# Performance work log

Hardware: AMD Instinct MI355X
Metric: run time of the kernel (lower is better)

The kernel has to match this reference:

```python
import jax, jax.numpy as jnp
import numpy as np

# Static config (matches init_kwargs)
B, T, D = 4, 2048, 1024
E = 8            # num_experts
K = 2            # top_k
S = 1            # num_shared_experts
H = 1408         # expert_hidden_dim = round_to(4*1024//(K+S), 64)
N = B * T        # 8192 tokens
CAPACITY = 2560  # ceil(1.25 * K * N / E)
AUX_COEF = 0.01


def setup_inputs() -> dict:
    key = jax.random.key(0)
    ks = jax.random.split(key, 6)
    s = 1024 ** -0.5
    return {
        "x": jax.random.normal(ks[0], (B, T, D), jnp.float32),
        "router_weight": jax.random.normal(ks[1], (E, D), jnp.float32) * 0.02,
        "w_fc": jax.random.normal(ks[2], (E, D, H), jnp.float32) * s,
        "w_proj": jax.random.normal(ks[3], (E, H, D), jnp.float32) * s,
        "ws_fc": jax.random.normal(ks[4], (S, D, H), jnp.float32) * s,
        "ws_proj": jax.random.normal(ks[5], (S, H, D), jnp.float32) * s,
    }


def reference(x, router_weight, w_fc, w_proj, ws_fc, ws_proj):
    x_flat = x.reshape(N, D)

    # Shared experts: relu(x @ ws_fc)^2 @ ws_proj, summed over S experts
    h_s = jnp.square(jax.nn.relu(jnp.einsum("nd,sdh->snh", x_flat, ws_fc)))
    shared_out = jnp.einsum("snh,shd->nd", h_s, ws_proj)

    # Router: softmax in fp32, top-k, renormalize
    router_logits = x_flat @ router_weight.T                 # [N, E]
    routing_probs = jax.nn.softmax(router_logits.astype(jnp.float32), axis=-1)
    topk_probs, topk_idx = jax.lax.top_k(routing_probs, K)   # [N, K]
    topk_probs = topk_probs / (jnp.sum(topk_probs, axis=-1, keepdims=True) + 1e-9)
    topk_probs = topk_probs.astype(x.dtype)

    # Aux load-balancing loss (f uses top-1 assignment, no grad)
    f = jax.lax.stop_gradient(
        jnp.mean(jax.nn.one_hot(topk_idx[:, 0], E, dtype=routing_probs.dtype), axis=0))
    p = jnp.mean(routing_probs, axis=0)
    aux_loss = AUX_COEF * float(E) * jnp.sum(f * p)

    # Capacity-based dispatch: stable sort assignments by expert id
    flat_idx = topk_idx.reshape(-1)                          # [N*K]
    flat_probs = topk_probs.reshape(-1)                      # [N*K]
    flat_tok = jnp.repeat(jnp.arange(N, dtype=jnp.int32), K)  # [N*K]
    order = jnp.argsort(flat_idx, stable=True)
    sorted_idx = flat_idx[order]
    sorted_tok = flat_tok[order]
    sorted_probs = flat_probs[order]

    counts = jnp.zeros((E,), jnp.int32).at[flat_idx].add(1)
    starts = jnp.concatenate([jnp.zeros((1,), jnp.int32), jnp.cumsum(counts[:-1])])
    pos_within = jnp.arange(N * K, dtype=jnp.int32) - starts[sorted_idx]
    keep = (pos_within < CAPACITY).astype(x.dtype)
    pos_clamped = jnp.minimum(pos_within, CAPACITY - 1)
    slot = sorted_idx * CAPACITY + pos_clamped               # [N*K] -> E*CAPACITY buffer

    # Scatter tokens into per-expert capacity buffers (dropped tokens zeroed by keep)
    expert_inputs = jnp.zeros((E * CAPACITY, D), x.dtype).at[slot].add(
        x_flat[sorted_tok] * keep[:, None])
    expert_inputs = expert_inputs.reshape(E, CAPACITY, D)

    # Grouped expert FFN: relu(.)^2 MLP per expert
    hidden = jnp.square(jax.nn.relu(jnp.einsum("ecd,edh->ech", expert_inputs, w_fc)))
    expert_output = jnp.einsum("ech,ehd->ecd", hidden, w_proj).reshape(E * CAPACITY, D)

    # Gather + weighted scatter-combine back to tokens
    gathered = expert_output[slot]                           # [N*K, D]
    weighted = gathered * (sorted_probs * keep)[:, None]
    routed_out = jnp.zeros((N, D), x.dtype).at[sorted_tok].add(weighted)

    y = (routed_out + shared_out).reshape(B, T, D)
    return y, aux_loss
```

## Files before the change

### kernel.cpp

```cpp
#include <hip/hip_runtime.h>


#define NTOK 8192
#define DDIM 1024
#define HDIM 1408
#define CAP  2560
#define NROWS (NTOK + 8*CAP)
#define YN   8388608

typedef __bf16 bf16x8 __attribute__((ext_vector_type(8)));
typedef float  f32x4  __attribute__((ext_vector_type(4)));

typedef __attribute__((address_space(1))) void gvoid_t;
typedef __attribute__((address_space(3))) void svoid_t;

static __device__ __forceinline__ void load_lds16(const void* g, void* l) {
  __builtin_amdgcn_global_load_lds((gvoid_t*)g, (svoid_t*)l, 16, 0, 0);
}

__global__ __launch_bounds__(256) void zero_kernel(float* __restrict__ y) {
  size_t idx = (size_t)blockIdx.x * 256 + threadIdx.x;
  float4 z = make_float4(0.f, 0.f, 0.f, 0.f);
  float4* p = (float4*)y;
#pragma unroll
  for (int j = 0; j < 4; ++j) p[idx + (size_t)j * 524288] = z;
}

__global__ __launch_bounds__(256) void tconv2_kernel(
    const float* __restrict__ in, __bf16* __restrict__ out,
    const float* __restrict__ in_s, __bf16* __restrict__ out_s, int R, int C) {
  __shared__ float t[64][33];
  int z = blockIdx.z, tid = threadIdx.x;
  const float* ip = (z < 8) ? in + (size_t)z * R * C : in_s;
  __bf16* op = (z < 8) ? out + (size_t)z * R * C : out_s;
  int c0 = blockIdx.x * 32, r0 = blockIdx.y * 64;
  int tx = tid & 31, ty = tid >> 5;
#pragma unroll
  for (int k = 0; k < 8; ++k)
    t[ty + k * 8][tx] = ip[(size_t)(r0 + ty + k * 8) * C + c0 + tx];
  __syncthreads();
  int cl = tid >> 3, rq = (tid & 7) * 8;
  bf16x8 o;
#pragma unroll
  for (int j = 0; j < 8; ++j) o[j] = (__bf16)t[rq + j][cl];
  *(bf16x8*)(op + (size_t)(c0 + cl) * R + r0 + rq) = o;
}

__global__ __launch_bounds__(256) void router_kernel(
    const float* __restrict__ x, const float* __restrict__ rw,
    __bf16* __restrict__ xbf,
    int2* __restrict__ e01, float2* __restrict__ p01,
    int* __restrict__ tok_row, float* __restrict__ scale_row,
    float* __restrict__ psum_part, int* __restrict__ fcnt_part) {
  __shared__ float rwl[8 * 1024];
  __shared__ float ps[8];
  __shared__ int fc[8];
  int tid = threadIdx.x;
  if (tid < 8) { ps[tid] = 0.f; fc[tid] = 0; }
  float4* rl4 = (float4*)rwl;
  const float4* rg4 = (const float4*)rw;
#pragma unroll
  for (int j = 0; j < 8; ++j) rl4[tid + 256 * j] = rg4[tid + 256 * j];
  __syncthreads();
  int lane = tid & 63, wid = tid >> 6;
  for (int it = 0; it < 8; ++it) {
    int t = blockIdx.x * 32 + wid * 8 + it;
    const float4* xt = (const float4*)(x + (size_t)t * DDIM);
    float a[8];
#pragma unroll
    for (int e = 0; e < 8; ++e) a[e] = 0.f;
    float4 v[4];
#pragma unroll
    for (int jj = 0; jj < 4; ++jj) {
      v[jj] = xt[lane * 4 + jj];
#pragma unroll
      for (int e = 0; e < 8; ++e) {
        float4 w = rl4[e * 256 + lane * 4 + jj];
        a[e] += v[jj].x * w.x + v[jj].y * w.y + v[jj].z * w.z + v[jj].w * w.w;
      }
    }
    {
      bf16x8 o0, o1;
#pragma unroll
      for (int jj = 0; jj < 2; ++jj) {
        o0[jj * 4 + 0] = (__bf16)v[jj].x; o0[jj * 4 + 1] = (__bf16)v[jj].y;
        o0[jj * 4 + 2] = (__bf16)v[jj].z; o0[jj * 4 + 3] = (__bf16)v[jj].w;
        o1[jj * 4 + 0] = (__bf16)v[jj + 2].x; o1[jj * 4 + 1] = (__bf16)v[jj + 2].y;
        o1[jj * 4 + 2] = (__bf16)v[jj + 2].z; o1[jj * 4 + 3] = (__bf16)v[jj + 2].w;
      }
      __bf16* xo = xbf + (size_t)t * DDIM + lane * 16;
      *(bf16x8*)xo = o0;
      *(bf16x8*)(xo + 8) = o1;
    }
#pragma unroll
    for (int off = 32; off >= 1; off >>= 1)
#pragma unroll
      for (int e = 0; e < 8; ++e) a[e] += __shfl_xor(a[e], off);
    if (lane == 0) {
      int am = 0; float m = a[0];
      for (int e = 1; e < 8; ++e) if (a[e] > m) { m = a[e]; am = e; }
      float s = 0.f, ex[8];
      for (int e = 0; e < 8; ++e) { ex[e] = expf(a[e] - m); s += ex[e]; }
      float inv = 1.f / s;
      int am2 = -1; float m2 = -3.4e38f;
      for (int e = 0; e < 8; ++e) if (e != am && a[e] > m2) { m2 = a[e]; am2 = e; }
      float p0 = ex[am] * inv, p1 = ex[am2] * inv;
      float rn = 1.f / (p0 + p1 + 1e-9f);
      e01[t] = make_int2(am, am2);
      p01[t] = make_float2(p0 * rn, p1 * rn);
      tok_row[t] = t;
      scale_row[t] = 1.f;
      atomicAdd(&fc[am], 1);
      for (int e = 0; e < 8; ++e) atomicAdd(&ps[e], ex[e] * inv);
    }
  }
  __syncthreads();
  if (tid < 8) { psum_part[blockIdx.x * 8 + tid] = ps[tid]; fcnt_part[blockIdx.x * 8 + tid] = fc[tid]; }
}

__global__ __launch_bounds__(256) void dispatch_kernel(
    const int2* __restrict__ e01, const float2* __restrict__ p01,
    int* __restrict__ tok_row, float* __restrict__ scale_row, int* __restrict__ counts,
    const float* __restrict__ psum_part, const int* __restrict__ fcnt_part,
    float* __restrict__ aux_out) {
  __shared__ int lcnt[256][8];
  __shared__ float aps[8];
  __shared__ int afc[8];
  int tid = threadIdx.x;
  if (tid < 8) {
    float s = 0.f; int c = 0;
    for (int i = 0; i < 256; ++i) { s += psum_part[i * 8 + tid]; c += fcnt_part[i * 8 + tid]; }
    aps[tid] = s; afc[tid] = c;
  }
  int my[8];
#pragma unroll
  for (int e = 0; e < 8; ++e) my[e] = 0;
  int base = tid * 64;
  for (int j = 0; j < 64; ++j) {
    int ent = base + j; int t = ent >> 1;
    int2 ee = e01[t];
    int ex = (ent & 1) ? ee.y : ee.x;
    my[ex]++;
  }
#pragma unroll
  for (int e = 0; e < 8; ++e) lcnt[tid][e] = my[e];
  __syncthreads();
  if (tid < 8) {
    int run = 0;
    for (int i = 0; i < 256; ++i) { int c = lcnt[i][tid]; lcnt[i][tid] = run; run += c; }
    counts[tid] = run < CAP ? run : CAP;
  }
  __syncthreads();
  int offs[8];
#pragma unroll
  for (int e = 0; e < 8; ++e) offs[e] = lcnt[tid][e];
  for (int j = 0; j < 64; ++j) {
    int ent = base + j; int t = ent >> 1; int k = ent & 1;
    int2 ee = e01[t];
    int ex = k ? ee.y : ee.x;
    float pr = k ? p01[t].y : p01[t].x;
    int pos = offs[ex]++;
    if (pos < CAP) {
      int row = NTOK + ex * CAP + pos;
      tok_row[row] = t;
      scale_row[row] = pr;
    }
  }
  if (tid == 0) {
    float s = 0.f;
    for (int e = 0; e < 8; ++e) s += ((float)afc[e] / 8192.f) * (aps[e] / 8192.f);
    *aux_out = 0.08f * s;
  }
}

template <int KD, int NDT, bool GATHER, int EPI>
__global__ __launch_bounds__(256, 4) void gemm_kernel(
    const __bf16* __restrict__ A, const __bf16* __restrict__ B,
    __bf16* __restrict__ Hout, float* __restrict__ Yout,
    const int* __restrict__ counts, const int* __restrict__ tok_row,
    const float* __restrict__ scale_row) {
  constexpr int NCT = NDT / 128;
  constexpr int SH = NTOK / 128;
  constexpr int ET = CAP / 128;
  int nwg = gridDim.x;
  int lin = (blockIdx.x & 7) * (nwg >> 3) + (blockIdx.x >> 3);
  int rem = lin % (4 * NCT);
  int rt = (lin / (4 * NCT)) * 4 + (rem & 3);
  int ct = rem >> 2;

  int g, i0, rowbase;
  if (rt < SH) { g = 8; rowbase = 0; i0 = rt << 7; }
  else { int r = rt - SH; g = r / ET; i0 = (r % ET) << 7; rowbase = NTOK + g * CAP; }
  int cnt = (g == 8) ? NTOK : counts[g];
  if (i0 >= cnt) return;

  __shared__ __align__(16) __bf16 As[128 * 64];
  __shared__ __align__(16) __bf16 Bs[128 * 64];
  __shared__ int   toksL[128];
  __shared__ float sclL[128];

  int tid = threadIdx.x, lane = tid & 63, wid = tid >> 6;

  if (tid < 128) {
    int i = i0 + tid; if (i > cnt - 1) i = cnt - 1;
    toksL[tid] = tok_row[rowbase + i];
    if (EPI == 2) sclL[tid] = scale_row[rowbase + i];
  }
  __syncthreads();

  int rsub = lane >> 3, csub = lane & 7;
  int csw = (csub ^ rsub) * 16;
  const char* aP[4];
  const char* bP[4];
  const char* Bg = (const char*)B + (size_t)g * NDT * KD * 2;
#pragma unroll
  for (int t = 0; t < 4; ++t) {
    int ia = wid * 32 + t * 8 + rsub;
    size_t arow = GATHER ? (size_t)toksL[ia] : (size_t)(rowbase + i0 + ia);
    aP[t] = (const char*)A + arow * (size_t)(KD * 2) + csw;
    int ib = ct * 128 + wid * 32 + t * 8 + rsub;
    bP[t] = Bg + (size_t)ib * (KD * 2) + csw;
  }

  f32x4 acc[4][4];
#pragma unroll
  for (int m2 = 0; m2 < 4; ++m2)
#pragma unroll
    for (int n2 = 0; n2 < 4; ++n2) acc[m2][n2] = f32x4{0.f, 0.f, 0.f, 0.f};

  int wr = wid >> 1, wc = wid & 1;
  int rA[4], rB[4], cS[2];
#pragma unroll
  for (int m2 = 0; m2 < 4; ++m2) rA[m2] = (wr * 64 + m2 * 16 + (lane & 15)) * 64;
#pragma unroll
  for (int n2 = 0; n2 < 4; ++n2) rB[n2] = (wc * 64 + n2 * 16 + (lane & 15)) * 64;
#pragma unroll
  for (int kk = 0; kk < 2; ++kk) cS[kk] = ((kk * 4 + (lane >> 4)) ^ (lane & 7)) * 8;

  for (int k0 = 0; k0 < KD; k0 += 64) {
    size_t kb = (size_t)k0 * 2;
#pragma unroll
    for (int t = 0; t < 4; ++t) {
      load_lds16(aP[t] + kb, &As[(wid * 32 + t * 8) * 64]);
      load_lds16(bP[t] + kb, &Bs[(wid * 32 + t * 8) * 64]);
    }
    __syncthreads();
#pragma unroll
    for (int kk = 0; kk < 2; ++kk) {
      bf16x8 af[4], bfr[4];
#pragma unroll
      for (int m2 = 0; m2 < 4; ++m2) af[m2] = *(const bf16x8*)&As[rA[m2] + cS[kk]];
#pragma unroll
      for (int n2 = 0; n2 < 4; ++n2) bfr[n2] = *(const bf16x8*)&Bs[rB[n2] + cS[kk]];
#pragma unroll
      for (int m2 = 0; m2 < 4; ++m2)
#pragma unroll
        for (int n2 = 0; n2 < 4; ++n2)
          acc[m2][n2] = __builtin_amdgcn_mfma_f32_16x16x32_bf16(af[m2], bfr[n2], acc[m2][n2], 0, 0, 0);
    }
    __syncthreads();
  }

#pragma unroll
  for (int m2 = 0; m2 < 4; ++m2) {
    int rb = wr * 64 + m2 * 16 + ((lane >> 4) << 2);
#pragma unroll
    for (int n2 = 0; n2 < 4; ++n2) {
      int col = ct * 128 + wc * 64 + n2 * 16 + (lane & 15);
#pragma unroll
      for (int r = 0; r < 4; ++r) {
        int grow = i0 + rb + r;
        if (grow < cnt) {
          float v = acc[m2][n2][r];
          if constexpr (EPI == 1) {
            v = fmaxf(v, 0.f);
            Hout[(size_t)(rowbase + grow) * NDT + col] = (__bf16)(v * v);
          } else {
            atomicAdd(&Yout[(size_t)toksL[rb + r] * NDT + col], v * sclL[rb + r]);
          }
        }
      }
    }
  }
}

extern "C" void kernel_launch(void* const* d_in, const int* in_sizes, int n_in,
                              void* d_out, int out_size, void* d_ws, size_t ws_size,
                              hipStream_t stream) {
  const float* x      = (const float*)d_in[0];
  const float* rw     = (const float*)d_in[1];
  const float* wfc    = (const float*)d_in[2];
  const float* wproj  = (const float*)d_in[3];
  const float* wsfc   = (const float*)d_in[4];
  const float* wsproj = (const float*)d_in[5];
  float* y = (float*)d_out;

  char* ws = (char*)d_ws;
  size_t off = 0;
  auto alloc = [&](size_t bytes) {
    void* p = ws + off;
    off += (bytes + 1023) & ~(size_t)1023;
    return p;
  };
  __bf16* xbf      = (__bf16*)alloc((size_t)NTOK * DDIM * 2);
  __bf16* B1       = (__bf16*)alloc((size_t)9 * HDIM * DDIM * 2);
  __bf16* B2       = (__bf16*)alloc((size_t)9 * DDIM * HDIM * 2);
  __bf16* H        = (__bf16*)alloc((size_t)NROWS * HDIM * 2);
  int*    tok_row  = (int*)alloc((size_t)NROWS * 4);
  float*  scale_row= (float*)alloc((size_t)NROWS * 4);
  int2*   e01      = (int2*)alloc((size_t)NTOK * 8);
  float2* p01      = (float2*)alloc((size_t)NTOK * 8);
  int*    counts   = (int*)alloc(1024);
  float*  psum_part= (float*)alloc(256 * 8 * 4);
  int*    fcnt_part= (int*)alloc(256 * 8 * 4);
  (void)ws_size; (void)out_size; (void)in_sizes; (void)n_in;

  zero_kernel<<<2048, 256, 0, stream>>>(y);
  tconv2_kernel<<<dim3(44, 16, 9), 256, 0, stream>>>(
      wfc, B1, wsfc, B1 + (size_t)8 * HDIM * DDIM, 1024, 1408);
  tconv2_kernel<<<dim3(32, 22, 9), 256, 0, stream>>>(
      wproj, B2, wsproj, B2 + (size_t)8 * DDIM * HDIM, 1408, 1024);
  router_kernel<<<256, 256, 0, stream>>>(x, rw, xbf, e01, p01, tok_row, scale_row,
                                         psum_part, fcnt_part);
  dispatch_kernel<<<1, 256, 0, stream>>>(e01, p01, tok_row, scale_row, counts,
                                         psum_part, fcnt_part, y + YN);
  gemm_kernel<1024, 1408, true, 1><<<2464, 256, 0, stream>>>(
      xbf, B1, H, nullptr, counts, tok_row, scale_row);
  gemm_kernel<1408, 1024, false, 2><<<1792, 256, 0, stream>>>(
      H, B2, nullptr, y, counts, tok_row, scale_row);
}
```

Measured before the change: 320.7 us.

## Double-buffer GEMM LDS tiles with K=32 steps and prefetch next tile

Replaces the single-buffered 64-wide K-step GEMM loop with a double-buffered shared-memory scheme using 32-wide K steps. The global-to-LDS loads for the next tile are issued before computing the current one, so only one barrier per iteration is needed. The swizzle and load layout are reorganized to match. The intent is to overlap memory latency with MFMA work. In exchange, the loop runs twice as many iterations, each doing half the math, and the swizzle changes bank-conflict behavior.

```diff
diff --git a/kernel.cpp b/kernel.cpp
--- a/kernel.cpp
+++ b/kernel.cpp
@@ -180,6 +180,7 @@
     const int* __restrict__ counts, const int* __restrict__ tok_row,
     const float* __restrict__ scale_row) {
   constexpr int NCT = NDT / 128;
+  constexpr int T = KD / 32;
   constexpr int SH = NTOK / 128;
   constexpr int ET = CAP / 128;
   int nwg = gridDim.x;
@@ -194,8 +195,7 @@
   int cnt = (g == 8) ? NTOK : counts[g];
   if (i0 >= cnt) return;
 
-  __shared__ __align__(16) __bf16 As[128 * 64];
-  __shared__ __align__(16) __bf16 Bs[128 * 64];
+  __shared__ __align__(16) __bf16 Sm[2][256 * 32];
   __shared__ int   toksL[128];
   __shared__ float sclL[128];
 
@@ -208,18 +208,22 @@
   }
   __syncthreads();
 
-  int rsub = lane >> 3, csub = lane & 7;
-  int csw = (csub ^ rsub) * 16;
-  const char* aP[4];
-  const char* bP[4];
+  const char* gsrc[4];
+  int ldsoff[4];
+  int rsub = lane >> 2, chunk = lane & 3;
   const char* Bg = (const char*)B + (size_t)g * NDT * KD * 2;
 #pragma unroll
-  for (int t = 0; t < 4; ++t) {
-    int ia = wid * 32 + t * 8 + rsub;
-    size_t arow = GATHER ? (size_t)toksL[ia] : (size_t)(rowbase + i0 + ia);
-    aP[t] = (const char*)A + arow * (size_t)(KD * 2) + csw;
-    int ib = ct * 128 + wid * 32 + t * 8 + rsub;
-    bP[t] = Bg + (size_t)ib * (KD * 2) + csw;
+  for (int q = 0; q < 4; ++q) {
+    int j = wid * 4 + q;
+    int row = (j & 7) * 16 + rsub;
+    int csw = (chunk ^ ((row >> 1) & 3)) * 16;
+    if (j < 8) {
+      size_t arow = GATHER ? (size_t)toksL[row] : (size_t)(rowbase + i0 + row);
+      gsrc[q] = (const char*)A + arow * (size_t)(KD * 2) + csw;
+    } else {
+      gsrc[q] = Bg + (size_t)(ct * 128 + row) * (KD * 2) + csw;
+    }
+    ldsoff[q] = j * 1024;
   }
 
   f32x4 acc[4][4];
@@ -229,35 +233,44 @@
     for (int n2 = 0; n2 < 4; ++n2) acc[m2][n2] = f32x4{0.f, 0.f, 0.f, 0.f};
 
   int wr = wid >> 1, wc = wid & 1;
-  int rA[4], rB[4], cS[2];
-#pragma unroll
-  for (int m2 = 0; m2 < 4; ++m2) rA[m2] = (wr * 64 + m2 * 16 + (lane & 15)) * 64;
-#pragma unroll
-  for (int n2 = 0; n2 < 4; ++n2) rB[n2] = (wc * 64 + n2 * 16 + (lane & 15)) * 64;
-#pragma unroll
-  for (int kk = 0; kk < 2; ++kk) cS[kk] = ((kk * 4 + (lane >> 4)) ^ (lane & 7)) * 8;
-
-  for (int k0 = 0; k0 < KD; k0 += 64) {
-    size_t kb = (size_t)k0 * 2;
-#pragma unroll
-    for (int t = 0; t < 4; ++t) {
-      load_lds16(aP[t] + kb, &As[(wid * 32 + t * 8) * 64]);
-      load_lds16(bP[t] + kb, &Bs[(wid * 32 + t * 8) * 64]);
-    }
-    __syncthreads();
-#pragma unroll
-    for (int kk = 0; kk < 2; ++kk) {
-      bf16x8 af[4], bfr[4];
-#pragma unroll
-      for (int m2 = 0; m2 < 4; ++m2) af[m2] = *(const bf16x8*)&As[rA[m2] + cS[kk]];
-#pragma unroll
-      for (int n2 = 0; n2 < 4; ++n2) bfr[n2] = *(const bf16x8*)&Bs[rB[n2] + cS[kk]];
-#pragma unroll
-      for (int m2 = 0; m2 < 4; ++m2)
-#pragma unroll
-        for (int n2 = 0; n2 < 4; ++n2)
-          acc[m2][n2] = __builtin_amdgcn_mfma_f32_16x16x32_bf16(af[m2], bfr[n2], acc[m2][n2], 0, 0, 0);
-    }
+  int rdA[4], rdB[4];
+#pragma unroll
+  for (int m2 = 0; m2 < 4; ++m2) {
+    int row = wr * 64 + m2 * 16 + (lane & 15);
+    rdA[m2] = row * 64 + (((lane >> 4) ^ ((row >> 1) & 3)) * 16);
+  }
+#pragma unroll
+  for (int n2 = 0; n2 < 4; ++n2) {
+    int row = wc * 64 + n2 * 16 + (lane & 15);
+    rdB[n2] = (128 + row) * 64 + (((lane >> 4) ^ ((row >> 1) & 3)) * 16);
+  }
+
+  auto stage = [&](int buf, int t) {
+#pragma unroll
+    for (int q = 0; q < 4; ++q)
+      load_lds16(gsrc[q] + (size_t)t * 64, (char*)&Sm[buf][0] + ldsoff[q]);
+  };
+  auto compute = [&](int buf) {
+    const char* Sb = (const char*)&Sm[buf][0];
+    bf16x8 af[4], bfr[4];
+#pragma unroll
+    for (int m2 = 0; m2 < 4; ++m2) af[m2] = *(const bf16x8*)(Sb + rdA[m2]);
+#pragma unroll
+    for (int n2 = 0; n2 < 4; ++n2) bfr[n2] = *(const bf16x8*)(Sb + rdB[n2]);
+#pragma unroll
+    for (int m2 = 0; m2 < 4; ++m2)
+#pragma unroll
+      for (int n2 = 0; n2 < 4; ++n2)
+        acc[m2][n2] = __builtin_amdgcn_mfma_f32_16x16x32_bf16(af[m2], bfr[n2], acc[m2][n2], 0, 0, 0);
+  };
+
+  stage(0, 0);
+  __syncthreads();
+#pragma unroll 2
+  for (int t = 0; t < T; ++t) {
+    if (t + 1 < T) stage((t + 1) & 1, t + 1);
+    __builtin_amdgcn_sched_barrier(0);
+    compute(t & 1);
     __syncthreads();
   }
 
```

Result: slower. 356.0 us (+11.0%).
